# Performance work log

Measured on AMD Instinct MI355X. Metric: run time of the kernel, lower is better.

The kernel has to match this reference:

```python
import jax, jax.numpy as jnp
import numpy as np

BATCH = 65536
HID = 256      # hidden_dim
DIN = 256      # input_dim == out_dim
R_MAX = 1.0
R_MIN = 0.0
MAX_PHASE = 6.28


def setup_inputs() -> dict:
    key = jax.random.key(0)
    ks = jax.random.split(key, 10)
    x_real = jax.random.normal(ks[0], (BATCH, HID), dtype=jnp.float32)
    x_imag = jax.random.normal(ks[1], (BATCH, HID), dtype=jnp.float32)
    u_k = jax.random.normal(ks[2], (BATCH, DIN), dtype=jnp.float32)
    # nu_log / theta_log: eigenvalues on a ring in the complex plane
    u1 = jax.random.uniform(ks[3], (HID,))
    nu_log = jnp.log(-0.5 * jnp.log(u1 * (R_MAX ** 2 - R_MIN ** 2) + R_MIN ** 2))
    u2 = jax.random.uniform(ks[4], (HID,))
    theta_log = jnp.log(MAX_PHASE * u2)
    diag_lambda = jnp.exp(-jnp.exp(nu_log) + 1j * jnp.exp(theta_log))
    gamma_log = jnp.log(jnp.sqrt(1 - jnp.abs(diag_lambda) ** 2))
    B_real = jax.random.normal(ks[5], (DIN, HID)) / jnp.sqrt(2 * HID)
    B_img = jax.random.normal(ks[6], (DIN, HID)) / jnp.sqrt(2 * HID)
    C_real = jax.random.normal(ks[7], (HID, DIN)) / jnp.sqrt(DIN)
    C_img = jax.random.normal(ks[8], (HID, DIN)) / jnp.sqrt(DIN)
    D = jax.random.normal(ks[9], (DIN,)) / jnp.sqrt(2 * DIN)
    return {
        "x_real": x_real, "x_imag": x_imag, "u_k": u_k,
        "nu_log": nu_log.astype(jnp.float32),
        "theta_log": theta_log.astype(jnp.float32),
        "gamma_log": gamma_log.astype(jnp.float32),
        "B_real": B_real.astype(jnp.float32), "B_img": B_img.astype(jnp.float32),
        "C_real": C_real.astype(jnp.float32), "C_img": C_img.astype(jnp.float32),
        "D": D.astype(jnp.float32),
    }


def reference(x_real, x_imag, u_k, nu_log, theta_log, gamma_log,
              B_real, B_img, C_real, C_img, D):
    # Lambda: diagonal complex recurrence eigenvalues, shape [HID]
    Lambda = jnp.exp(-jnp.exp(nu_log) + 1j * jnp.exp(theta_log))
    gamma = jnp.exp(gamma_log)  # [HID]
    # B_norm = (B_real + i B_img) * gamma ; input projection, [DIN, HID]
    # u_k is real, so u @ B_norm = (u @ (B_real*gamma)) + i (u @ (B_img*gamma))
    uB_r = u_k @ (B_real * gamma[None, :])
    uB_i = u_k @ (B_img * gamma[None, :])
    x_km1 = x_real + 1j * x_imag  # [BATCH, HID] complex state
    x_k = Lambda[None, :] * x_km1 + (uB_r + 1j * uB_i)
    # y = Re(x_k @ C) + D*u ; Re((a+ib)(Cr+iCi)) = a@Cr - b@Ci
    y_k = x_k.real @ C_real - x_k.imag @ C_img + D[None, :] * u_k
    return (x_k.real, x_k.imag, y_k)
```

## Files before the change

### kernel.cpp

```cpp
#include <hip/hip_runtime.h>

typedef __attribute__((ext_vector_type(8))) short short8;
typedef __attribute__((ext_vector_type(4))) float f32x4;

#define HID 256
#define BATCH 65536

__device__ inline ushort bf16u(float f) {
  unsigned u = __builtin_bit_cast(unsigned, f);
  u = (u + 0x7FFFu + ((u >> 16) & 1u)) >> 16;
  return (ushort)u;
}
__device__ inline unsigned packbf2(float a, float b) {
  unsigned ua = __builtin_bit_cast(unsigned, a);
  unsigned ub = __builtin_bit_cast(unsigned, b);
  ua = (ua + 0x7FFFu + ((ua >> 16) & 1u)) >> 16;
  ub = (ub + 0x7FFFu + ((ub >> 16) & 1u)) >> 16;
  return ua | (ub << 16);
}
__device__ inline short8 cvt8(float4 a, float4 b) {
  union { short8 v; unsigned u[4]; } r;
  r.u[0] = packbf2(a.x, a.y);
  r.u[1] = packbf2(a.z, a.w);
  r.u[2] = packbf2(b.x, b.y);
  r.u[3] = packbf2(b.z, b.w);
  return r.v;
}

__global__ void prep_lambda(const float* __restrict__ nu, const float* __restrict__ th,
                            float* __restrict__ lam) {
  int i = threadIdx.x;
  float mag = __expf(-__expf(nu[i]));
  float ang = __expf(th[i]);
  lam[i] = mag * __cosf(ang);
  lam[HID + i] = mag * __sinf(ang);
}

__global__ void prep_weights(const float* __restrict__ gl, const float* __restrict__ Br,
                             const float* __restrict__ Bi, const float* __restrict__ Cr,
                             const float* __restrict__ Ci, ushort* __restrict__ wbr,
                             ushort* __restrict__ wbi, ushort* __restrict__ wcc) {
  int t = blockIdx.x * 256 + threadIdx.x;
  int lane = t & 63;
  int l15 = lane & 15, quad = lane >> 4;
  union { ushort s[8]; uint4 q; } r;
  if (t < 16384) {
    const float* B = (t < 8192) ? Br : Bi;
    ushort* w = (t < 8192) ? wbr : wbi;
    int e = t & 8191;
    int ntile = e >> 9;
    int ks = (e >> 6) & 7;
    int n = ntile * 16 + l15;
    int k0 = ks * 32 + quad * 8;
    float g = __expf(gl[n]);
#pragma unroll
    for (int j = 0; j < 8; ++j) r.s[j] = bf16u(B[(k0 + j) * HID + n] * g);
    *(uint4*)(w + (size_t)e * 8) = r.q;
  } else {
    int e = t - 16384;
    int ntile = e >> 10;
    int ks = (e >> 6) & 15;
    int n = ntile * 16 + l15;
    int k0 = ks * 32 + quad * 8;
#pragma unroll
    for (int j = 0; j < 8; ++j) {
      int k = k0 + j;
      float v = (k < 256) ? Cr[k * HID + n] : -Ci[(k - 256) * HID + n];
      r.s[j] = bf16u(v);
    }
    *(uint4*)(wcc + (size_t)e * 8) = r.q;
  }
}

__global__ __launch_bounds__(256, 2) void lru_main(
    const float* __restrict__ xr_in, const float* __restrict__ xi_in,
    const float* __restrict__ u_in, const float* __restrict__ Dv,
    const float* __restrict__ lam, const ushort* __restrict__ wbr,
    const ushort* __restrict__ wbi, const ushort* __restrict__ wcc,
    float* __restrict__ out) {
  __shared__ ushort xk[64 * 520];

  const int tid = threadIdx.x;
  const int lane = tid & 63;
  const int wave = tid >> 6;
  const int l15 = lane & 15;
  const int quad = lane >> 4;
  const int row0 = blockIdx.x << 6;
  const int col0 = wave << 6;

  f32x4 accR[4][4], accI[4][4];
#pragma unroll
  for (int i = 0; i < 4; ++i)
#pragma unroll
    for (int j = 0; j < 4; ++j)
#pragma unroll
      for (int r = 0; r < 4; ++r) { accR[i][j][r] = 0.f; accI[i][j][r] = 0.f; }

  for (int ks = 0; ks < 8; ++ks) {
    short8 a[4];
#pragma unroll
    for (int rt = 0; rt < 4; ++rt) {
      const float* up = u_in + (size_t)(row0 + rt * 16 + l15) * HID + (ks * 32 + quad * 8);
      float4 f0 = *(const float4*)up;
      float4 f1 = *(const float4*)(up + 4);
      a[rt] = cvt8(f0, f1);
    }
    short8 br[4], bi[4];
#pragma unroll
    for (int ct = 0; ct < 4; ++ct) {
      int off = (((wave * 4 + ct) * 8 + ks) * 64 + lane) * 8;
      br[ct] = *(const short8*)(wbr + off);
      bi[ct] = *(const short8*)(wbi + off);
    }
#pragma unroll
    for (int rt = 0; rt < 4; ++rt)
#pragma unroll
      for (int ct = 0; ct < 4; ++ct) {
        accR[rt][ct] = __builtin_amdgcn_mfma_f32_16x16x32_bf16(a[rt], br[ct], accR[rt][ct], 0, 0, 0);
        accI[rt][ct] = __builtin_amdgcn_mfma_f32_16x16x32_bf16(a[rt], bi[ct], accI[rt][ct], 0, 0, 0);
      }
  }

  float lr[4], li[4], dd[4];
#pragma unroll
  for (int ct = 0; ct < 4; ++ct) {
    int n = col0 + ct * 16 + l15;
    lr[ct] = lam[n];
    li[ct] = lam[HID + n];
    dd[ct] = Dv[n];
  }
  f32x4 accY[4][4];
#pragma unroll
  for (int rt = 0; rt < 4; ++rt)
#pragma unroll
    for (int ct = 0; ct < 4; ++ct) {
      int n = col0 + ct * 16 + l15;
#pragma unroll
      for (int r = 0; r < 4; ++r) {
        int m = rt * 16 + quad * 4 + r;
        int idx = (row0 + m) * HID + n;
        float xr = xr_in[idx];
        float xi = xi_in[idx];
        float nr = lr[ct] * xr - li[ct] * xi + accR[rt][ct][r];
        float ni = lr[ct] * xi + li[ct] * xr + accI[rt][ct][r];
        out[idx] = nr;
        out[16777216 + idx] = ni;
        accY[rt][ct][r] = dd[ct] * u_in[idx];
        xk[m * 520 + n] = bf16u(nr);
        xk[m * 520 + 256 + n] = bf16u(ni);
      }
    }
  __syncthreads();

  for (int ks = 0; ks < 16; ++ks) {
    short8 a[4];
#pragma unroll
    for (int rt = 0; rt < 4; ++rt)
      a[rt] = *(const short8*)&xk[(rt * 16 + l15) * 520 + ks * 32 + quad * 8];
    short8 b[4];
#pragma unroll
    for (int ct = 0; ct < 4; ++ct) {
      int off = (((wave * 4 + ct) * 16 + ks) * 64 + lane) * 8;
      b[ct] = *(const short8*)(wcc + off);
    }
#pragma unroll
    for (int rt = 0; rt < 4; ++rt)
#pragma unroll
      for (int ct = 0; ct < 4; ++ct)
        accY[rt][ct] = __builtin_amdgcn_mfma_f32_16x16x32_bf16(a[rt], b[ct], accY[rt][ct], 0, 0, 0);
  }
#pragma unroll
  for (int rt = 0; rt < 4; ++rt)
#pragma unroll
    for (int ct = 0; ct < 4; ++ct) {
      int n = col0 + ct * 16 + l15;
#pragma unroll
      for (int r = 0; r < 4; ++r) {
        int m = rt * 16 + quad * 4 + r;
        int idx = (row0 + m) * HID + n;
        out[33554432 + idx] = accY[rt][ct][r];
      }
    }
}

extern "C" void kernel_launch(void* const* d_in, const int* in_sizes, int n_in,
                              void* d_out, int out_size, void* d_ws, size_t ws_size,
                              hipStream_t stream) {
  const float* x_real = (const float*)d_in[0];
  const float* x_imag = (const float*)d_in[1];
  const float* u_k = (const float*)d_in[2];
  const float* nu_log = (const float*)d_in[3];
  const float* theta_log = (const float*)d_in[4];
  const float* gamma_log = (const float*)d_in[5];
  const float* B_real = (const float*)d_in[6];
  const float* B_img = (const float*)d_in[7];
  const float* C_real = (const float*)d_in[8];
  const float* C_img = (const float*)d_in[9];
  const float* Dv = (const float*)d_in[10];

  float* lam = (float*)d_ws;
  ushort* wbr = (ushort*)d_ws + 1024;
  ushort* wbi = wbr + 65536;
  ushort* wcc = wbi + 65536;

  prep_lambda<<<1, 256, 0, stream>>>(nu_log, theta_log, lam);
  prep_weights<<<128, 256, 0, stream>>>(gamma_log, B_real, B_img, C_real, C_img, wbr, wbi, wcc);
  lru_main<<<BATCH / 64, 256, 0, stream>>>(x_real, x_imag, u_k, Dv, lam, wbr, wbi, wcc,
                                           (float*)d_out);
}
```

Measured before the change: 421.3 us.

## Use 8 waves per block with narrower column tiles, nontemporal IO, merged prep kernels

The main kernel now runs 512 threads (8 waves) per 64-row block, and each wave covers 32 columns instead of 64. This halves per-wave accumulator registers and should raise occupancy, but each wave now re-reads and re-converts the full u tile, doubling that global read and conversion work. The streamed x inputs and all outputs use nontemporal loads and stores to avoid polluting cache. The two small prep kernels are merged into one launch to remove a kernel launch.

```diff
diff --git a/kernel.cpp b/kernel.cpp
--- a/kernel.cpp
+++ b/kernel.cpp
@@ -5,6 +5,7 @@
 
 #define HID 256
 #define BATCH 65536
+#define XSTR 520
 
 __device__ inline ushort bf16u(float f) {
   unsigned u = __builtin_bit_cast(unsigned, f);
@@ -27,19 +28,20 @@
   return r.v;
 }
 
-__global__ void prep_lambda(const float* __restrict__ nu, const float* __restrict__ th,
-                            float* __restrict__ lam) {
-  int i = threadIdx.x;
-  float mag = __expf(-__expf(nu[i]));
-  float ang = __expf(th[i]);
-  lam[i] = mag * __cosf(ang);
-  lam[HID + i] = mag * __sinf(ang);
-}
-
-__global__ void prep_weights(const float* __restrict__ gl, const float* __restrict__ Br,
-                             const float* __restrict__ Bi, const float* __restrict__ Cr,
-                             const float* __restrict__ Ci, ushort* __restrict__ wbr,
-                             ushort* __restrict__ wbi, ushort* __restrict__ wcc) {
+__global__ void prep_all(const float* __restrict__ nu, const float* __restrict__ th,
+                         const float* __restrict__ gl, const float* __restrict__ Br,
+                         const float* __restrict__ Bi, const float* __restrict__ Cr,
+                         const float* __restrict__ Ci, float* __restrict__ lam,
+                         ushort* __restrict__ wbr, ushort* __restrict__ wbi,
+                         ushort* __restrict__ wcc) {
+  if (blockIdx.x == 128) {
+    int i = threadIdx.x;
+    float mag = __expf(-__expf(nu[i]));
+    float ang = __expf(th[i]);
+    lam[i] = mag * __cosf(ang);
+    lam[HID + i] = mag * __sinf(ang);
+    return;
+  }
   int t = blockIdx.x * 256 + threadIdx.x;
   int lane = t & 63;
   int l15 = lane & 15, quad = lane >> 4;
@@ -72,13 +74,13 @@
   }
 }
 
-__global__ __launch_bounds__(256, 2) void lru_main(
+__global__ __launch_bounds__(512, 4) void lru_main(
     const float* __restrict__ xr_in, const float* __restrict__ xi_in,
     const float* __restrict__ u_in, const float* __restrict__ Dv,
     const float* __restrict__ lam, const ushort* __restrict__ wbr,
     const ushort* __restrict__ wbi, const ushort* __restrict__ wcc,
     float* __restrict__ out) {
-  __shared__ ushort xk[64 * 520];
+  __shared__ ushort xk[64 * XSTR];
 
   const int tid = threadIdx.x;
   const int lane = tid & 63;
@@ -86,13 +88,13 @@
   const int l15 = lane & 15;
   const int quad = lane >> 4;
   const int row0 = blockIdx.x << 6;
-  const int col0 = wave << 6;
-
-  f32x4 accR[4][4], accI[4][4];
+  const int col0 = wave << 5;
+
+  f32x4 accR[4][2], accI[4][2];
 #pragma unroll
   for (int i = 0; i < 4; ++i)
 #pragma unroll
-    for (int j = 0; j < 4; ++j)
+    for (int j = 0; j < 2; ++j)
 #pragma unroll
       for (int r = 0; r < 4; ++r) { accR[i][j][r] = 0.f; accI[i][j][r] = 0.f; }
 
@@ -105,49 +107,49 @@
       float4 f1 = *(const float4*)(up + 4);
       a[rt] = cvt8(f0, f1);
     }
-    short8 br[4], bi[4];
-#pragma unroll
-    for (int ct = 0; ct < 4; ++ct) {
-      int off = (((wave * 4 + ct) * 8 + ks) * 64 + lane) * 8;
+    short8 br[2], bi[2];
+#pragma unroll
+    for (int ct = 0; ct < 2; ++ct) {
+      int off = (((wave * 2 + ct) * 8 + ks) * 64 + lane) * 8;
       br[ct] = *(const short8*)(wbr + off);
       bi[ct] = *(const short8*)(wbi + off);
     }
 #pragma unroll
     for (int rt = 0; rt < 4; ++rt)
 #pragma unroll
-      for (int ct = 0; ct < 4; ++ct) {
+      for (int ct = 0; ct < 2; ++ct) {
         accR[rt][ct] = __builtin_amdgcn_mfma_f32_16x16x32_bf16(a[rt], br[ct], accR[rt][ct], 0, 0, 0);
         accI[rt][ct] = __builtin_amdgcn_mfma_f32_16x16x32_bf16(a[rt], bi[ct], accI[rt][ct], 0, 0, 0);
       }
   }
 
-  float lr[4], li[4], dd[4];
-#pragma unroll
-  for (int ct = 0; ct < 4; ++ct) {
+  float lr[2], li[2], dd[2];
+#pragma unroll
+  for (int ct = 0; ct < 2; ++ct) {
     int n = col0 + ct * 16 + l15;
     lr[ct] = lam[n];
     li[ct] = lam[HID + n];
     dd[ct] = Dv[n];
   }
-  f32x4 accY[4][4];
+  f32x4 accY[4][2];
 #pragma unroll
   for (int rt = 0; rt < 4; ++rt)
 #pragma unroll
-    for (int ct = 0; ct < 4; ++ct) {
+    for (int ct = 0; ct < 2; ++ct) {
       int n = col0 + ct * 16 + l15;
 #pragma unroll
       for (int r = 0; r < 4; ++r) {
         int m = rt * 16 + quad * 4 + r;
         int idx = (row0 + m) * HID + n;
-        float xr = xr_in[idx];
-        float xi = xi_in[idx];
+        float xr = __builtin_nontemporal_load(&xr_in[idx]);
+        float xi = __builtin_nontemporal_load(&xi_in[idx]);
         float nr = lr[ct] * xr - li[ct] * xi + accR[rt][ct][r];
         float ni = lr[ct] * xi + li[ct] * xr + accI[rt][ct][r];
-        out[idx] = nr;
-        out[16777216 + idx] = ni;
+        __builtin_nontemporal_store(nr, &out[idx]);
+        __builtin_nontemporal_store(ni, &out[16777216 + idx]);
         accY[rt][ct][r] = dd[ct] * u_in[idx];
-        xk[m * 520 + n] = bf16u(nr);
-        xk[m * 520 + 256 + n] = bf16u(ni);
+        xk[m * XSTR + n] = bf16u(nr);
+        xk[m * XSTR + 256 + n] = bf16u(ni);
       }
     }
   __syncthreads();
@@ -156,29 +158,29 @@
     short8 a[4];
 #pragma unroll
     for (int rt = 0; rt < 4; ++rt)
-      a[rt] = *(const short8*)&xk[(rt * 16 + l15) * 520 + ks * 32 + quad * 8];
-    short8 b[4];
-#pragma unroll
-    for (int ct = 0; ct < 4; ++ct) {
-      int off = (((wave * 4 + ct) * 16 + ks) * 64 + lane) * 8;
+      a[rt] = *(const short8*)&xk[(rt * 16 + l15) * XSTR + ks * 32 + quad * 8];
+    short8 b[2];
+#pragma unroll
+    for (int ct = 0; ct < 2; ++ct) {
+      int off = (((wave * 2 + ct) * 16 + ks) * 64 + lane) * 8;
       b[ct] = *(const short8*)(wcc + off);
     }
 #pragma unroll
     for (int rt = 0; rt < 4; ++rt)
 #pragma unroll
-      for (int ct = 0; ct < 4; ++ct)
+      for (int ct = 0; ct < 2; ++ct)
         accY[rt][ct] = __builtin_amdgcn_mfma_f32_16x16x32_bf16(a[rt], b[ct], accY[rt][ct], 0, 0, 0);
   }
 #pragma unroll
   for (int rt = 0; rt < 4; ++rt)
 #pragma unroll
-    for (int ct = 0; ct < 4; ++ct) {
+    for (int ct = 0; ct < 2; ++ct) {
       int n = col0 + ct * 16 + l15;
 #pragma unroll
       for (int r = 0; r < 4; ++r) {
         int m = rt * 16 + quad * 4 + r;
         int idx = (row0 + m) * HID + n;
-        out[33554432 + idx] = accY[rt][ct][r];
+        __builtin_nontemporal_store(accY[rt][ct][r], &out[33554432 + idx]);
       }
     }
 }
@@ -203,8 +205,8 @@
   ushort* wbi = wbr + 65536;
   ushort* wcc = wbi + 65536;
 
-  prep_lambda<<<1, 256, 0, stream>>>(nu_log, theta_log, lam);
-  prep_weights<<<128, 256, 0, stream>>>(gamma_log, B_real, B_img, C_real, C_img, wbr, wbi, wcc);
-  lru_main<<<BATCH / 64, 256, 0, stream>>>(x_real, x_imag, u_k, Dv, lam, wbr, wbi, wcc,
+  prep_all<<<129, 256, 0, stream>>>(nu_log, theta_log, gamma_log, B_real, B_img,
+                                    C_real, C_img, lam, wbr, wbi, wcc);
+  lru_main<<<BATCH / 64, 512, 0, stream>>>(x_real, x_imag, u_k, Dv, lam, wbr, wbi, wcc,
                                            (float*)d_out);
 }
```

Measured after the change: 459.2 us. 1.09x slower.
